# Performance work log

Hardware: AMD Instinct MI355X
Metric: run time of the kernel (lower is better)

The kernel has to match this reference:

```python
import jax, jax.numpy as jnp
import numpy as np

FP8_MAX = 448.0  # finfo(float8_e4m3fn).max

def setup_inputs() -> dict:
    key = jax.random.key(0)
    k_x, k_w, k_b = jax.random.split(key, 3)
    B, S, D_IN, D_OUT = 4, 2048, 4096, 16384
    x = jax.random.normal(k_x, (B, S, D_IN), dtype=jnp.float32)
    # Build an fp8-quantized weight exactly as FP8WeightOnlyLinear.from_linear does:
    w = jax.random.normal(k_w, (D_OUT, D_IN), dtype=jnp.float32) * 0.02
    amax = jnp.max(jnp.abs(w))
    scale = jnp.where(amax > 0, amax / FP8_MAX, 1.0)
    # round-trip through float8_e4m3fn so stored values are true fp8 codes
    w_fp8 = jnp.clip(w / scale, -FP8_MAX, FP8_MAX).astype(jnp.float8_e4m3fn)
    weight_fp8 = w_fp8.astype(jnp.float32)  # fp8-representable values, held in fp32
    weight_scale = scale.reshape(1).astype(jnp.float32)
    bias = jax.random.normal(k_b, (D_OUT,), dtype=jnp.float32) * 0.01
    return {"x": x, "weight_fp8": weight_fp8, "weight_scale": weight_scale, "bias": bias}

def reference(x, weight_fp8, weight_scale, bias):
    # w = weight_fp8.to(x.dtype) * weight_scale ; out = x @ w.T + bias
    w = weight_fp8.astype(x.dtype) * weight_scale.astype(x.dtype)  # [D_OUT, D_IN]
    out = jnp.einsum('bsd,od->bso', x, w) + bias.astype(x.dtype)
    return out
```

## Files before the change

### kernel.cpp

```cpp
#include <hip/hip_runtime.h>
#include <stdint.h>

typedef unsigned int u32;
using i32x4 = __attribute__((ext_vector_type(4))) int;

#define GLD_LDS16(SRC, DST)                                      \
  __builtin_amdgcn_global_load_lds(                              \
      (const __attribute__((address_space(1))) void*)(SRC),      \
      (__attribute__((address_space(3))) void*)(DST), 16, 0, 0)

#define SCHED0() __builtin_amdgcn_sched_barrier(0)
#define BAR()    __builtin_amdgcn_s_barrier()
#define PRIO(x)  __builtin_amdgcn_s_setprio(x)

__global__ __launch_bounds__(256)
void quant_rows(const float* __restrict__ x, const float* __restrict__ w,
                signed char* __restrict__ xq, signed char* __restrict__ wq,
                float* __restrict__ sx, float* __restrict__ sw,
                int Mrows, int totRows, int K) {
  __shared__ float red[4];
  for (int row = blockIdx.x; row < totRows; row += gridDim.x) {
    const bool isx = row < Mrows;
    const float* src = isx ? x + (size_t)row * K : w + (size_t)(row - Mrows) * K;
    const float4* s4 = reinterpret_cast<const float4*>(src) + threadIdx.x * 4;
    float4 v[4];
#pragma unroll
    for (int g = 0; g < 4; ++g) v[g] = s4[g];
    float am = 0.f;
#pragma unroll
    for (int g = 0; g < 4; ++g)
      am = fmaxf(am, fmaxf(fmaxf(fabsf(v[g].x), fabsf(v[g].y)),
                           fmaxf(fabsf(v[g].z), fabsf(v[g].w))));
#pragma unroll
    for (int m = 1; m <= 32; m <<= 1) am = fmaxf(am, __shfl_xor(am, m));
    if ((threadIdx.x & 63) == 0) red[threadIdx.x >> 6] = am;
    __syncthreads();
    am = fmaxf(fmaxf(red[0], red[1]), fmaxf(red[2], red[3]));
    const float s   = am > 0.f ? am * (1.f / 127.f) : 1.f;
    const float inv = am > 0.f ? 127.f / am : 0.f;
    u32 pk[4];
#pragma unroll
    for (int g = 0; g < 4; ++g) {
      const float* vp = reinterpret_cast<const float*>(&v[g]);
      u32 p = 0;
#pragma unroll
      for (int e = 0; e < 4; ++e) {
        int q = (int)rintf(vp[e] * inv);
        q = q < -127 ? -127 : (q > 127 ? 127 : q);
        p |= ((u32)(q & 0xff)) << (8 * e);
      }
      pk[g] = p;
    }
    signed char* dst = (isx ? xq + (size_t)row * K : wq + (size_t)(row - Mrows) * K)
                       + threadIdx.x * 16;
    *reinterpret_cast<uint4*>(dst) = make_uint4(pk[0], pk[1], pk[2], pk[3]);
    if (threadIdx.x == 0) { if (isx) sx[row] = s; else sw[row - Mrows] = s; }
    __syncthreads();
  }
}

__global__ __launch_bounds__(512, 2)
void gemm_i8_bk128(const signed char* __restrict__ A,
                   const signed char* __restrict__ B,
                   const float* __restrict__ sx,
                   const float* __restrict__ sw,
                   const float* __restrict__ wscale_p,
                   const float* __restrict__ bias,
                   float* __restrict__ C,
                   int Nn, int Kk, int NT) {
  __shared__ signed char lds[2][2][256 * 128];

  const int tid  = threadIdx.x;
  const int lane = tid & 63;
  const int wave = tid >> 6;
  const int wr = wave >> 2;
  const int wc = wave & 3;

  const int bid = blockIdx.x;
  const int cpx = gridDim.x >> 3;
  const int wg  = (bid & 7) * cpx + (bid >> 3);
  const int mt = wg / NT, nt = wg % NT;
  const int m0 = mt * 256, n0 = nt * 256;

  const int srow = lane >> 3;
  const int ss   = (lane & 7) ^ (srow & 7);
  const int r16  = lane & 15;
  const int kq   = lane >> 4;

  const signed char* ga = A + ((size_t)m0 + wave * 32 + srow) * Kk + ss * 16;
  const signed char* gb = B + ((size_t)n0 + wave * 32 + srow) * Kk + ss * 16;

  const int aoff = (wr * 128 + r16) * 128 + ((kq ^ (r16 & 7)) << 4);
  const int boff = (wc * 64  + r16) * 128 + ((kq ^ (r16 & 7)) << 4);

  i32x4 acc[8][4];
#pragma unroll
  for (int i = 0; i < 8; ++i)
#pragma unroll
    for (int j = 0; j < 4; ++j)
      acc[i][j] = (i32x4){0, 0, 0, 0};

  i32x4 afA[4], afB[4];
  i32x4 bP[4], bQ[4];

#define STAGE128(bfi_, op_, kt_) do {                                           \
    const signed char* _g = ((op_) ? gb : ga) + (size_t)(kt_) * 128;            \
    signed char* _d = &lds[bfi_][op_][wave * 32 * 128];                         \
    GLD_LDS16(_g,                    _d);                                       \
    GLD_LDS16(_g + (size_t)8  * Kk,  _d + 1024);                                \
    GLD_LDS16(_g + (size_t)16 * Kk,  _d + 2048);                                \
    GLD_LDS16(_g + (size_t)24 * Kk,  _d + 3072);                                \
  } while (0)

#define LDFA(AF_, la_, mh_, ks_) do {                                           \
    _Pragma("unroll") for (int _i = 0; _i < 4; ++_i)                            \
      AF_[_i] = *reinterpret_cast<const i32x4*>(                                \
          (la_) + ((aoff + ((mh_) * 4 + _i) * 2048) ^ ((ks_) << 6)));           \
  } while (0)

#define LDFB(BF_, lb_, ks_) do {                                                \
    _Pragma("unroll") for (int _n = 0; _n < 4; ++_n)                            \
      BF_[_n] = *reinterpret_cast<const i32x4*>(                                \
          (lb_) + ((boff + _n * 2048) ^ ((ks_) << 6)));                         \
  } while (0)

#define MFMAC(mh_, AF_, BF_)                                                    \
  _Pragma("unroll") for (int i = 0; i < 4; ++i)                                 \
  _Pragma("unroll") for (int n = 0; n < 4; ++n)                                 \
    acc[(mh_) * 4 + i][n] = __builtin_amdgcn_mfma_i32_16x16x64_i8(              \
        AF_[i], BF_[n], acc[(mh_) * 4 + i][n], 0, 0, 0)

  const int KT = Kk >> 7;

  STAGE128(0, 0, 0); STAGE128(0, 1, 0);
  STAGE128(1, 0, 1); STAGE128(1, 1, 1);
  asm volatile("s_waitcnt vmcnt(8)" ::: "memory");
  SCHED0(); BAR(); SCHED0();
  LDFA(afA, (const signed char*)&lds[0][0][0], 0, 0);
  LDFB(bP,  (const signed char*)&lds[0][1][0], 0);
  LDFB(bQ,  (const signed char*)&lds[0][1][0], 1);

#define TILE128(t_, CUR_) do {                                                  \
    const signed char* laC = &lds[CUR_][0][0];                                  \
    const signed char* laN = &lds[(CUR_) ^ 1][0][0];                            \
    const signed char* lbN = &lds[(CUR_) ^ 1][1][0];                            \
    const int kt2 = ((t_) + 2 < KT) ? (t_) + 2 : KT - 1;                        \
                                                                        \
    SCHED0(); BAR(); SCHED0();                                                  \
    LDFA(afB, laC, 1, 0);                                                       \
    PRIO(1); MFMAC(0, afA, bP); PRIO(0);                       \
    LDFA(afA, laC, 0, 1);                                                       \
    STAGE128(CUR_, 1, kt2);                                                     \
    PRIO(1); MFMAC(1, afB, bP); PRIO(0);                       \
    LDFA(afB, laC, 1, 1);                                                       \
    SCHED0();                                                                   \
    asm volatile("s_waitcnt vmcnt(4)" ::: "memory");                            \
                                                                        \
    SCHED0(); BAR(); SCHED0();                                                  \
    PRIO(1); MFMAC(0, afA, bQ); PRIO(0);                       \
    LDFA(afA, laN, 0, 0);                                                       \
    LDFB(bP, lbN, 0);                                                           \
    STAGE128(CUR_, 0, kt2);                                                     \
    PRIO(1); MFMAC(1, afB, bQ); PRIO(0);                       \
    LDFB(bQ, lbN, 1);                                \
  } while (0)

  for (int t = 0; t < KT; t += 2) {
    TILE128(t,     0);
    TILE128(t + 1, 1);
  }

  const float wsc = wscale_p[0];
  float cw[4], bv[4];
#pragma unroll
  for (int ni = 0; ni < 4; ++ni) {
    const int col = n0 + wc * 64 + ni * 16 + r16;
    cw[ni] = sw[col] * wsc;
    bv[ni] = bias[col];
  }
#pragma unroll
  for (int mi = 0; mi < 8; ++mi) {
#pragma unroll
    for (int r = 0; r < 4; ++r) {
      const int row = m0 + wr * 128 + mi * 16 + kq * 4 + r;
      const float sxr = sx[row];
      float* cp = C + (size_t)row * Nn + (n0 + wc * 64 + r16);
#pragma unroll
      for (int ni = 0; ni < 4; ++ni)
        cp[ni * 16] = (float)acc[mi][ni][r] * (sxr * cw[ni]) + bv[ni];
    }
  }
#undef STAGE128
#undef LDFA
#undef LDFB
#undef MFMAC
#undef TILE128
}

extern "C" void kernel_launch(void* const* d_in, const int* in_sizes, int n_in,
                              void* d_out, int out_size, void* d_ws, size_t ws_size,
                              hipStream_t stream) {
  (void)n_in; (void)out_size; (void)ws_size;
  const float* x  = (const float*)d_in[0];
  const float* w  = (const float*)d_in[1];
  const float* sc = (const float*)d_in[2];
  const float* bs = (const float*)d_in[3];
  float* out = (float*)d_out;

  const int N = in_sizes[3];
  const int K = in_sizes[1] / N;
  const int M = in_sizes[0] / K;

  signed char* xq = (signed char*)d_ws;
  signed char* wq = xq + (size_t)M * K;
  float* sxp = (float*)(wq + (size_t)N * K);
  float* swp = sxp + M;

  quant_rows<<<M + N, 256, 0, stream>>>(x, w, xq, wq, sxp, swp, M, M + N, K);

  const int NT = N / 256;
  const int nwg = (M / 256) * NT;
  gemm_i8_bk128<<<nwg, 512, 0, stream>>>(xq, wq, sxp, swp, sc, bs, out, N, K, NT);
}
```

Baseline: 629.0 us.

## Replace interleaved LDS/MFMA ping-pong with bulk fragment read then MFMA burst

The GEMM main loop drops the fine-grained interleaving of LDS fragment reads, MFMA groups, global-to-LDS staging and priority toggles. Each K-tile now reads all 24 A/B fragments up front, issues all 64 MFMAs in one burst, and then stages the next tiles with a single barrier per tile. This cuts barriers and setprio overhead and simplifies scheduling. In exchange it holds more registers for fragments and loses overlap between LDS reads and MFMA within a wave, so it relies on the two co-resident workgroups to hide latency.

Result: slower. 644.4 us (+2.4%).

```diff
diff --git a/kernel.cpp b/kernel.cpp
--- a/kernel.cpp
+++ b/kernel.cpp
@@ -11,7 +11,6 @@
 
 #define SCHED0() __builtin_amdgcn_sched_barrier(0)
 #define BAR()    __builtin_amdgcn_s_barrier()
-#define PRIO(x)  __builtin_amdgcn_s_setprio(x)
 
 __global__ __launch_bounds__(256)
 void quant_rows(const float* __restrict__ x, const float* __restrict__ w,
@@ -60,14 +59,14 @@
 }
 
 __global__ __launch_bounds__(512, 2)
-void gemm_i8_bk128(const signed char* __restrict__ A,
-                   const signed char* __restrict__ B,
-                   const float* __restrict__ sx,
-                   const float* __restrict__ sw,
-                   const float* __restrict__ wscale_p,
-                   const float* __restrict__ bias,
-                   float* __restrict__ C,
-                   int Nn, int Kk, int NT) {
+void gemm_i8_deep(const signed char* __restrict__ A,
+                  const signed char* __restrict__ B,
+                  const float* __restrict__ sx,
+                  const float* __restrict__ sw,
+                  const float* __restrict__ wscale_p,
+                  const float* __restrict__ bias,
+                  float* __restrict__ C,
+                  int Nn, int Kk, int NT) {
   __shared__ signed char lds[2][2][256 * 128];
 
   const int tid  = threadIdx.x;
@@ -100,8 +99,8 @@
     for (int j = 0; j < 4; ++j)
       acc[i][j] = (i32x4){0, 0, 0, 0};
 
-  i32x4 afA[4], afB[4];
-  i32x4 bP[4], bQ[4];
+  i32x4 af[16];
+  i32x4 bf[8];
 
 #define STAGE128(bfi_, op_, kt_) do {                                           \
     const signed char* _g = ((op_) ? gb : ga) + (size_t)(kt_) * 128;            \
@@ -112,62 +111,66 @@
     GLD_LDS16(_g + (size_t)24 * Kk,  _d + 3072);                                \
   } while (0)
 
-#define LDFA(AF_, la_, mh_, ks_) do {                                           \
-    _Pragma("unroll") for (int _i = 0; _i < 4; ++_i)                            \
-      AF_[_i] = *reinterpret_cast<const i32x4*>(                                \
-          (la_) + ((aoff + ((mh_) * 4 + _i) * 2048) ^ ((ks_) << 6)));           \
-  } while (0)
-
-#define LDFB(BF_, lb_, ks_) do {                                                \
-    _Pragma("unroll") for (int _n = 0; _n < 4; ++_n)                            \
-      BF_[_n] = *reinterpret_cast<const i32x4*>(                                \
-          (lb_) + ((boff + _n * 2048) ^ ((ks_) << 6)));                         \
-  } while (0)
-
-#define MFMAC(mh_, AF_, BF_)                                                    \
-  _Pragma("unroll") for (int i = 0; i < 4; ++i)                                 \
-  _Pragma("unroll") for (int n = 0; n < 4; ++n)                                 \
-    acc[(mh_) * 4 + i][n] = __builtin_amdgcn_mfma_i32_16x16x64_i8(              \
-        AF_[i], BF_[n], acc[(mh_) * 4 + i][n], 0, 0, 0)
+#define READ24(la_, lb_) do {                                                   \
+    const signed char* _la0 = (la_) + aoff;                                     \
+    const signed char* _la1 = (la_) + (aoff ^ 64);                              \
+    const signed char* _lb0 = (lb_) + boff;                                     \
+    const signed char* _lb1 = (lb_) + (boff ^ 64);                              \
+    _Pragma("unroll") for (int _n = 0; _n < 4; ++_n)                            \
+      bf[_n]      = *reinterpret_cast<const i32x4*>(_lb0 + _n * 2048);          \
+    _Pragma("unroll") for (int _i = 0; _i < 4; ++_i)                            \
+      af[_i]      = *reinterpret_cast<const i32x4*>(_la0 + _i * 2048);          \
+    _Pragma("unroll") for (int _i = 0; _i < 4; ++_i)                            \
+      af[4 + _i]  = *reinterpret_cast<const i32x4*>(_la0 + (4 + _i) * 2048);    \
+    _Pragma("unroll") for (int _n = 0; _n < 4; ++_n)                            \
+      bf[4 + _n]  = *reinterpret_cast<const i32x4*>(_lb1 + _n * 2048);          \
+    _Pragma("unroll") for (int _i = 0; _i < 4; ++_i)                            \
+      af[8 + _i]  = *reinterpret_cast<const i32x4*>(_la1 + _i * 2048);          \
+    _Pragma("unroll") for (int _i = 0; _i < 4; ++_i)                            \
+      af[12 + _i] = *reinterpret_cast<const i32x4*>(_la1 + (4 + _i) * 2048);    \
+  } while (0)
+
+#define MFMA64() do {                                                           \
+    _Pragma("unroll") for (int _i = 0; _i < 4; ++_i)                            \
+    _Pragma("unroll") for (int _n = 0; _n < 4; ++_n)                            \
+      acc[_i][_n] = __builtin_amdgcn_mfma_i32_16x16x64_i8(                      \
+          af[_i], bf[_n], acc[_i][_n], 0, 0, 0);                                \
+    _Pragma("unroll") for (int _i = 0; _i < 4; ++_i)                            \
+    _Pragma("unroll") for (int _n = 0; _n < 4; ++_n)                            \
+      acc[4 + _i][_n] = __builtin_amdgcn_mfma_i32_16x16x64_i8(                  \
+          af[4 + _i], bf[_n], acc[4 + _i][_n], 0, 0, 0);                        \
+    _Pragma("unroll") for (int _i = 0; _i < 4; ++_i)                            \
+    _Pragma("unroll") for (int _n = 0; _n < 4; ++_n)                            \
+      acc[_i][_n] = __builtin_amdgcn_mfma_i32_16x16x64_i8(                      \
+          af[8 + _i], bf[4 + _n], acc[_i][_n], 0, 0, 0);                        \
+    _Pragma("unroll") for (int _i = 0; _i < 4; ++_i)                            \
+    _Pragma("unroll") for (int _n = 0; _n < 4; ++_n)                            \
+      acc[4 + _i][_n] = __builtin_amdgcn_mfma_i32_16x16x64_i8(                  \
+          af[12 + _i], bf[4 + _n], acc[4 + _i][_n], 0, 0, 0);                   \
+  } while (0)
 
   const int KT = Kk >> 7;
 
   STAGE128(0, 0, 0); STAGE128(0, 1, 0);
   STAGE128(1, 0, 1); STAGE128(1, 1, 1);
   asm volatile("s_waitcnt vmcnt(8)" ::: "memory");
-  SCHED0(); BAR(); SCHED0();
-  LDFA(afA, (const signed char*)&lds[0][0][0], 0, 0);
-  LDFB(bP,  (const signed char*)&lds[0][1][0], 0);
-  LDFB(bQ,  (const signed char*)&lds[0][1][0], 1);
-
-#define TILE128(t_, CUR_) do {                                                  \
-    const signed char* laC = &lds[CUR_][0][0];                                  \
-    const signed char* laN = &lds[(CUR_) ^ 1][0][0];                            \
-    const signed char* lbN = &lds[(CUR_) ^ 1][1][0];                            \
+
+#define TILE(t_, CUR_) do {                                                     \
     const int kt2 = ((t_) + 2 < KT) ? (t_) + 2 : KT - 1;                        \
-                                                                        \
     SCHED0(); BAR(); SCHED0();                                                  \
-    LDFA(afB, laC, 1, 0);                                                       \
-    PRIO(1); MFMAC(0, afA, bP); PRIO(0);                       \
-    LDFA(afA, laC, 0, 1);                                                       \
+    READ24((const signed char*)&lds[CUR_][0][0],                                \
+           (const signed char*)&lds[CUR_][1][0]);                               \
+    SCHED0();                                                                   \
+    MFMA64();                                                                   \
+    SCHED0();                                                                   \
+    STAGE128(CUR_, 0, kt2);                                                     \
     STAGE128(CUR_, 1, kt2);                                                     \
-    PRIO(1); MFMAC(1, afB, bP); PRIO(0);                       \
-    LDFA(afB, laC, 1, 1);                                                       \
-    SCHED0();                                                                   \
-    asm volatile("s_waitcnt vmcnt(4)" ::: "memory");                            \
-                                                                        \
-    SCHED0(); BAR(); SCHED0();                                                  \
-    PRIO(1); MFMAC(0, afA, bQ); PRIO(0);                       \
-    LDFA(afA, laN, 0, 0);                                                       \
-    LDFB(bP, lbN, 0);                                                           \
-    STAGE128(CUR_, 0, kt2);                                                     \
-    PRIO(1); MFMAC(1, afB, bQ); PRIO(0);                       \
-    LDFB(bQ, lbN, 1);                                \
+    asm volatile("s_waitcnt vmcnt(8)" ::: "memory");   \
   } while (0)
 
   for (int t = 0; t < KT; t += 2) {
-    TILE128(t,     0);
-    TILE128(t + 1, 1);
+    TILE(t,     0);
+    TILE(t + 1, 1);
   }
 
   const float wsc = wscale_p[0];
@@ -191,10 +194,9 @@
     }
   }
 #undef STAGE128
-#undef LDFA
-#undef LDFB
-#undef MFMAC
-#undef TILE128
+#undef READ24
+#undef MFMA64
+#undef TILE
 }
 
 extern "C" void kernel_launch(void* const* d_in, const int* in_sizes, int n_in,
@@ -220,5 +222,5 @@
 
   const int NT = N / 256;
   const int nwg = (M / 256) * NT;
-  gemm_i8_bk128<<<nwg, 512, 0, stream>>>(xq, wq, sxp, swp, sc, bs, out, N, K, NT);
+  gemm_i8_deep<<<nwg, 512, 0, stream>>>(xq, wq, sxp, swp, sc, bs, out, N, K, NT);
 }
```

## Load B operand directly from global into registers, stage only A in LDS

Applied to the files above, without the earlier changes.

The GEMM now loads B fragments from global memory straight into registers, double-buffered across k-tiles, while only the A operand goes through LDS. This halves LDS footprint and LDS read traffic. The block-to-tile mapping is hardcoded so each XCD owns a band of N tiles with all 32 M tiles, and the s_setprio hints are removed. The risks are uncoalesced 16-byte global loads of B that are duplicated across the two wave rows. The mapping also assumes M/256=32 and N/256=64, so it only holds for this problem shape.

Result: slower. 995.6 us (+58.3%).

```diff
diff --git a/kernel.cpp b/kernel.cpp
--- a/kernel.cpp
+++ b/kernel.cpp
@@ -11,7 +11,6 @@
 
 #define SCHED0() __builtin_amdgcn_sched_barrier(0)
 #define BAR()    __builtin_amdgcn_s_barrier()
-#define PRIO(x)  __builtin_amdgcn_s_setprio(x)
 
 __global__ __launch_bounds__(256)
 void quant_rows(const float* __restrict__ x, const float* __restrict__ w,
@@ -60,15 +59,15 @@
 }
 
 __global__ __launch_bounds__(512, 2)
-void gemm_i8_bk128(const signed char* __restrict__ A,
-                   const signed char* __restrict__ B,
-                   const float* __restrict__ sx,
-                   const float* __restrict__ sw,
-                   const float* __restrict__ wscale_p,
-                   const float* __restrict__ bias,
-                   float* __restrict__ C,
-                   int Nn, int Kk, int NT) {
-  __shared__ signed char lds[2][2][256 * 128];
+void gemm_i8_bdir(const signed char* __restrict__ A,
+                  const signed char* __restrict__ B,
+                  const float* __restrict__ sx,
+                  const float* __restrict__ sw,
+                  const float* __restrict__ wscale_p,
+                  const float* __restrict__ bias,
+                  float* __restrict__ C,
+                  int Nn, int Kk) {
+  __shared__ signed char lds[2][256 * 128];
 
   const int tid  = threadIdx.x;
   const int lane = tid & 63;
@@ -77,9 +76,10 @@
   const int wc = wave & 3;
 
   const int bid = blockIdx.x;
-  const int cpx = gridDim.x >> 3;
-  const int wg  = (bid & 7) * cpx + (bid >> 3);
-  const int mt = wg / NT, nt = wg % NT;
+  const int xcd = bid & 7;
+  const int j   = bid >> 3;
+  const int nt  = xcd * 8 + (j >> 5);
+  const int mt  = j & 31;
   const int m0 = mt * 256, n0 = nt * 256;
 
   const int srow = lane >> 3;
@@ -88,86 +88,76 @@
   const int kq   = lane >> 4;
 
   const signed char* ga = A + ((size_t)m0 + wave * 32 + srow) * Kk + ss * 16;
-  const signed char* gb = B + ((size_t)n0 + wave * 32 + srow) * Kk + ss * 16;
+  const signed char* gBb = B + ((size_t)n0 + wc * 64 + r16) * Kk + (kq << 4);
 
   const int aoff = (wr * 128 + r16) * 128 + ((kq ^ (r16 & 7)) << 4);
-  const int boff = (wc * 64  + r16) * 128 + ((kq ^ (r16 & 7)) << 4);
 
   i32x4 acc[8][4];
 #pragma unroll
   for (int i = 0; i < 8; ++i)
 #pragma unroll
-    for (int j = 0; j < 4; ++j)
-      acc[i][j] = (i32x4){0, 0, 0, 0};
+    for (int jj = 0; jj < 4; ++jj)
+      acc[i][jj] = (i32x4){0, 0, 0, 0};
 
   i32x4 afA[4], afB[4];
-  i32x4 bP[4], bQ[4];
-
-#define STAGE128(bfi_, op_, kt_) do {                                           \
-    const signed char* _g = ((op_) ? gb : ga) + (size_t)(kt_) * 128;            \
-    signed char* _d = &lds[bfi_][op_][wave * 32 * 128];                         \
+  i32x4 bfP[8], bfQ[8];
+
+#define STAGEA(bfi_, kt_) do {                                                  \
+    const signed char* _g = ga + (size_t)(kt_) * 128;                           \
+    signed char* _d = &lds[bfi_][wave * 32 * 128];                              \
     GLD_LDS16(_g,                    _d);                                       \
     GLD_LDS16(_g + (size_t)8  * Kk,  _d + 1024);                                \
     GLD_LDS16(_g + (size_t)16 * Kk,  _d + 2048);                                \
     GLD_LDS16(_g + (size_t)24 * Kk,  _d + 3072);                                \
   } while (0)
 
+#define LOADB(BF_, kt_) do {                                                    \
+    const signed char* _b = gBb + (size_t)(kt_) * 128;                          \
+    _Pragma("unroll") for (int _n = 0; _n < 4; ++_n) {                          \
+      BF_[_n]     = *reinterpret_cast<const i32x4*>(_b + (size_t)(_n * 16) * Kk);      \
+      BF_[4 + _n] = *reinterpret_cast<const i32x4*>(_b + (size_t)(_n * 16) * Kk + 64); \
+    } } while (0)
+
 #define LDFA(AF_, la_, mh_, ks_) do {                                           \
     _Pragma("unroll") for (int _i = 0; _i < 4; ++_i)                            \
       AF_[_i] = *reinterpret_cast<const i32x4*>(                                \
           (la_) + ((aoff + ((mh_) * 4 + _i) * 2048) ^ ((ks_) << 6)));           \
   } while (0)
 
-#define LDFB(BF_, lb_, ks_) do {                                                \
-    _Pragma("unroll") for (int _n = 0; _n < 4; ++_n)                            \
-      BF_[_n] = *reinterpret_cast<const i32x4*>(                                \
-          (lb_) + ((boff + _n * 2048) ^ ((ks_) << 6)));                         \
+#define MFMAC(mh_, AF_, BF_, kb_)                                               \
+  _Pragma("unroll") for (int _i = 0; _i < 4; ++_i)                              \
+  _Pragma("unroll") for (int _n = 0; _n < 4; ++_n)                              \
+    acc[(mh_) * 4 + _i][_n] = __builtin_amdgcn_mfma_i32_16x16x64_i8(            \
+        AF_[_i], BF_[(kb_) * 4 + _n], acc[(mh_) * 4 + _i][_n], 0, 0, 0)
+
+  const int KT = Kk >> 7;
+
+  STAGEA(0, 0);
+  LOADB(bfP, 0);
+  STAGEA(1, 1);
+
+#define TILE(t_, CUR_, BF_, BFN_) do {                                          \
+    const signed char* laC = &lds[CUR_][0];                                     \
+    const int kt1 = ((t_) + 1 < KT) ? (t_) + 1 : KT - 1;                        \
+    const int kt2 = ((t_) + 2 < KT) ? (t_) + 2 : KT - 1;                        \
+    asm volatile("s_waitcnt vmcnt(4)" ::: "memory");      \
+    SCHED0(); BAR(); SCHED0();                                                  \
+    LOADB(BFN_, kt1);                             \
+    LDFA(afA, laC, 0, 0);                                                       \
+    MFMAC(0, afA, BF_, 0);                                     \
+    LDFA(afB, laC, 1, 0);                                                       \
+    MFMAC(1, afB, BF_, 0);                                     \
+    LDFA(afA, laC, 0, 1);                                                       \
+    MFMAC(0, afA, BF_, 1);                                     \
+    LDFA(afB, laC, 1, 1);                                                       \
+    MFMAC(1, afB, BF_, 1);                                     \
+    SCHED0(); BAR(); SCHED0();                      \
+    STAGEA(CUR_, kt2);                                  \
   } while (0)
 
-#define MFMAC(mh_, AF_, BF_)                                                    \
-  _Pragma("unroll") for (int i = 0; i < 4; ++i)                                 \
-  _Pragma("unroll") for (int n = 0; n < 4; ++n)                                 \
-    acc[(mh_) * 4 + i][n] = __builtin_amdgcn_mfma_i32_16x16x64_i8(              \
-        AF_[i], BF_[n], acc[(mh_) * 4 + i][n], 0, 0, 0)
-
-  const int KT = Kk >> 7;
-
-  STAGE128(0, 0, 0); STAGE128(0, 1, 0);
-  STAGE128(1, 0, 1); STAGE128(1, 1, 1);
-  asm volatile("s_waitcnt vmcnt(8)" ::: "memory");
-  SCHED0(); BAR(); SCHED0();
-  LDFA(afA, (const signed char*)&lds[0][0][0], 0, 0);
-  LDFB(bP,  (const signed char*)&lds[0][1][0], 0);
-  LDFB(bQ,  (const signed char*)&lds[0][1][0], 1);
-
-#define TILE128(t_, CUR_) do {                                                  \
-    const signed char* laC = &lds[CUR_][0][0];                                  \
-    const signed char* laN = &lds[(CUR_) ^ 1][0][0];                            \
-    const signed char* lbN = &lds[(CUR_) ^ 1][1][0];                            \
-    const int kt2 = ((t_) + 2 < KT) ? (t_) + 2 : KT - 1;                        \
-                                                                        \
-    SCHED0(); BAR(); SCHED0();                                                  \
-    LDFA(afB, laC, 1, 0);                                                       \
-    PRIO(1); MFMAC(0, afA, bP); PRIO(0);                       \
-    LDFA(afA, laC, 0, 1);                                                       \
-    STAGE128(CUR_, 1, kt2);                                                     \
-    PRIO(1); MFMAC(1, afB, bP); PRIO(0);                       \
-    LDFA(afB, laC, 1, 1);                                                       \
-    SCHED0();                                                                   \
-    asm volatile("s_waitcnt vmcnt(4)" ::: "memory");                            \
-                                                                        \
-    SCHED0(); BAR(); SCHED0();                                                  \
-    PRIO(1); MFMAC(0, afA, bQ); PRIO(0);                       \
-    LDFA(afA, laN, 0, 0);                                                       \
-    LDFB(bP, lbN, 0);                                                           \
-    STAGE128(CUR_, 0, kt2);                                                     \
-    PRIO(1); MFMAC(1, afB, bQ); PRIO(0);                       \
-    LDFB(bQ, lbN, 1);                                \
-  } while (0)
-
   for (int t = 0; t < KT; t += 2) {
-    TILE128(t,     0);
-    TILE128(t + 1, 1);
+    TILE(t,     0, bfP, bfQ);
+    TILE(t + 1, 1, bfQ, bfP);
   }
 
   const float wsc = wscale_p[0];
@@ -190,11 +180,11 @@
         cp[ni * 16] = (float)acc[mi][ni][r] * (sxr * cw[ni]) + bv[ni];
     }
   }
-#undef STAGE128
+#undef STAGEA
+#undef LOADB
 #undef LDFA
-#undef LDFB
 #undef MFMAC
-#undef TILE128
+#undef TILE
 }
 
 extern "C" void kernel_launch(void* const* d_in, const int* in_sizes, int n_in,
@@ -218,7 +208,6 @@
 
   quant_rows<<<M + N, 256, 0, stream>>>(x, w, xq, wq, sxp, swp, M, M + N, K);
 
-  const int NT = N / 256;
-  const int nwg = (M / 256) * NT;
-  gemm_i8_bk128<<<nwg, 512, 0, stream>>>(xq, wq, sxp, swp, sc, bs, out, N, K, NT);
+  const int nwg = (M / 256) * (N / 256);
+  gemm_i8_bdir<<<nwg, 512, 0, stream>>>(xq, wq, sxp, swp, sc, bs, out, N, K);
 }
```

## Shrink GEMM tile to 128x128 with 4-wave workgroups and rebalanced MFMA schedule

Applied to the files above, without the earlier changes.

Replaces the 256x256 tile, 8-wave int8 GEMM with a 128x128 tile, 4-wave kernel. Each wave keeps a 64x64 accumulator, and the in-loop schedule is reworked so MFMA batches interleave with LDS fragment loads and global-to-LDS staging. Smaller tiles halve LDS use per workgroup and give more workgroups. In exchange, arithmetic intensity per tile drops, which doubles global and L2 traffic for A and B.

Result: slower. 814.8 us (+29.5%).

```diff
diff --git a/kernel.cpp b/kernel.cpp
--- a/kernel.cpp
+++ b/kernel.cpp
@@ -59,28 +59,28 @@
   }
 }
 
-__global__ __launch_bounds__(512, 2)
-void gemm_i8_bk128(const signed char* __restrict__ A,
-                   const signed char* __restrict__ B,
-                   const float* __restrict__ sx,
-                   const float* __restrict__ sw,
-                   const float* __restrict__ wscale_p,
-                   const float* __restrict__ bias,
-                   float* __restrict__ C,
-                   int Nn, int Kk, int NT) {
-  __shared__ signed char lds[2][2][256 * 128];
+__global__ __launch_bounds__(256, 2)
+void gemm_i8_2wg(const signed char* __restrict__ A,
+                 const signed char* __restrict__ B,
+                 const float* __restrict__ sx,
+                 const float* __restrict__ sw,
+                 const float* __restrict__ wscale_p,
+                 const float* __restrict__ bias,
+                 float* __restrict__ C,
+                 int Nn, int Kk, int NT) {
+  __shared__ signed char lds[2][2][128 * 128];
 
   const int tid  = threadIdx.x;
   const int lane = tid & 63;
   const int wave = tid >> 6;
-  const int wr = wave >> 2;
-  const int wc = wave & 3;
+  const int wr = wave >> 1;
+  const int wc = wave & 1;
 
   const int bid = blockIdx.x;
   const int cpx = gridDim.x >> 3;
   const int wg  = (bid & 7) * cpx + (bid >> 3);
   const int mt = wg / NT, nt = wg % NT;
-  const int m0 = mt * 256, n0 = nt * 256;
+  const int m0 = mt * 128, n0 = nt * 128;
 
   const int srow = lane >> 3;
   const int ss   = (lane & 7) ^ (srow & 7);
@@ -90,12 +90,12 @@
   const signed char* ga = A + ((size_t)m0 + wave * 32 + srow) * Kk + ss * 16;
   const signed char* gb = B + ((size_t)n0 + wave * 32 + srow) * Kk + ss * 16;
 
-  const int aoff = (wr * 128 + r16) * 128 + ((kq ^ (r16 & 7)) << 4);
-  const int boff = (wc * 64  + r16) * 128 + ((kq ^ (r16 & 7)) << 4);
-
-  i32x4 acc[8][4];
-#pragma unroll
-  for (int i = 0; i < 8; ++i)
+  const int aoff = (wr * 64 + r16) * 128 + ((kq ^ (r16 & 7)) << 4);
+  const int boff = (wc * 64 + r16) * 128 + ((kq ^ (r16 & 7)) << 4);
+
+  i32x4 acc[4][4];
+#pragma unroll
+  for (int i = 0; i < 4; ++i)
 #pragma unroll
     for (int j = 0; j < 4; ++j)
       acc[i][j] = (i32x4){0, 0, 0, 0};
@@ -103,7 +103,7 @@
   i32x4 afA[4], afB[4];
   i32x4 bP[4], bQ[4];
 
-#define STAGE128(bfi_, op_, kt_) do {                                           \
+#define STAGE1(bfi_, op_, kt_) do {                                             \
     const signed char* _g = ((op_) ? gb : ga) + (size_t)(kt_) * 128;            \
     signed char* _d = &lds[bfi_][op_][wave * 32 * 128];                         \
     GLD_LDS16(_g,                    _d);                                       \
@@ -112,10 +112,10 @@
     GLD_LDS16(_g + (size_t)24 * Kk,  _d + 3072);                                \
   } while (0)
 
-#define LDFA(AF_, la_, mh_, ks_) do {                                           \
+#define LDFA(AF_, la_, ks_) do {                                                \
     _Pragma("unroll") for (int _i = 0; _i < 4; ++_i)                            \
       AF_[_i] = *reinterpret_cast<const i32x4*>(                                \
-          (la_) + ((aoff + ((mh_) * 4 + _i) * 2048) ^ ((ks_) << 6)));           \
+          (la_) + ((aoff + _i * 2048) ^ ((ks_) << 6)));                         \
   } while (0)
 
 #define LDFB(BF_, lb_, ks_) do {                                                \
@@ -124,50 +124,53 @@
           (lb_) + ((boff + _n * 2048) ^ ((ks_) << 6)));                         \
   } while (0)
 
-#define MFMAC(mh_, AF_, BF_)                                                    \
-  _Pragma("unroll") for (int i = 0; i < 4; ++i)                                 \
-  _Pragma("unroll") for (int n = 0; n < 4; ++n)                                 \
-    acc[(mh_) * 4 + i][n] = __builtin_amdgcn_mfma_i32_16x16x64_i8(              \
-        AF_[i], BF_[n], acc[(mh_) * 4 + i][n], 0, 0, 0)
+#define MFMA16(AF_, BF_)                                                        \
+  _Pragma("unroll") for (int _i = 0; _i < 4; ++_i)                              \
+  _Pragma("unroll") for (int _n = 0; _n < 4; ++_n)                              \
+    acc[_i][_n] = __builtin_amdgcn_mfma_i32_16x16x64_i8(                        \
+        AF_[_i], BF_[_n], acc[_i][_n], 0, 0, 0)
+
+#define MFMA8(AF_, BF_, nlo_)                                                   \
+  _Pragma("unroll") for (int _i = 0; _i < 4; ++_i)                              \
+  _Pragma("unroll") for (int _n = 0; _n < 2; ++_n)                              \
+    acc[_i][(nlo_) + _n] = __builtin_amdgcn_mfma_i32_16x16x64_i8(               \
+        AF_[_i], BF_[(nlo_) + _n], acc[_i][(nlo_) + _n], 0, 0, 0)
 
   const int KT = Kk >> 7;
 
-  STAGE128(0, 0, 0); STAGE128(0, 1, 0);
-  STAGE128(1, 0, 1); STAGE128(1, 1, 1);
+  STAGE1(0, 0, 0); STAGE1(0, 1, 0);
+  STAGE1(1, 0, 1); STAGE1(1, 1, 1);
   asm volatile("s_waitcnt vmcnt(8)" ::: "memory");
   SCHED0(); BAR(); SCHED0();
-  LDFA(afA, (const signed char*)&lds[0][0][0], 0, 0);
+  LDFA(afA, (const signed char*)&lds[0][0][0], 0);
   LDFB(bP,  (const signed char*)&lds[0][1][0], 0);
   LDFB(bQ,  (const signed char*)&lds[0][1][0], 1);
 
-#define TILE128(t_, CUR_) do {                                                  \
+#define TILE(t_, CUR_) do {                                                     \
     const signed char* laC = &lds[CUR_][0][0];                                  \
     const signed char* laN = &lds[(CUR_) ^ 1][0][0];                            \
     const signed char* lbN = &lds[(CUR_) ^ 1][1][0];                            \
     const int kt2 = ((t_) + 2 < KT) ? (t_) + 2 : KT - 1;                        \
                                                                         \
     SCHED0(); BAR(); SCHED0();                                                  \
-    LDFA(afB, laC, 1, 0);                                                       \
-    PRIO(1); MFMAC(0, afA, bP); PRIO(0);                       \
-    LDFA(afA, laC, 0, 1);                                                       \
-    STAGE128(CUR_, 1, kt2);                                                     \
-    PRIO(1); MFMAC(1, afB, bP); PRIO(0);                       \
-    LDFA(afB, laC, 1, 1);                                                       \
+    LDFA(afB, laC, 1);                                               \
+    STAGE1(CUR_, 1, kt2);                        \
+    PRIO(1); MFMA16(afA, bP); PRIO(0);                             \
     SCHED0();                                                                   \
-    asm volatile("s_waitcnt vmcnt(4)" ::: "memory");                            \
+    asm volatile("s_waitcnt vmcnt(4)" ::: "memory");       \
                                                                         \
     SCHED0(); BAR(); SCHED0();                                                  \
-    PRIO(1); MFMAC(0, afA, bQ); PRIO(0);                       \
-    LDFA(afA, laN, 0, 0);                                                       \
+    PRIO(1); MFMA8(afB, bQ, 0); PRIO(0);                   \
+    LDFA(afA, laN, 0);                                        \
     LDFB(bP, lbN, 0);                                                           \
-    STAGE128(CUR_, 0, kt2);                                                     \
-    PRIO(1); MFMAC(1, afB, bQ); PRIO(0);                       \
-    LDFB(bQ, lbN, 1);                                \
+    STAGE1(CUR_, 0, kt2);                                      \
+    PRIO(1); MFMA8(afB, bQ, 2); PRIO(0);                   \
+    LDFB(bQ, lbN, 1);                               \
   } while (0)
 
   for (int t = 0; t < KT; t += 2) {
-    TILE128(t,     0);
-    TILE128(t + 1, 1);
+    TILE(t,     0);
+    TILE(t + 1, 1);
   }
 
   const float wsc = wscale_p[0];
@@ -179,10 +182,10 @@
     bv[ni] = bias[col];
   }
 #pragma unroll
-  for (int mi = 0; mi < 8; ++mi) {
+  for (int mi = 0; mi < 4; ++mi) {
 #pragma unroll
     for (int r = 0; r < 4; ++r) {
-      const int row = m0 + wr * 128 + mi * 16 + kq * 4 + r;
+      const int row = m0 + wr * 64 + mi * 16 + kq * 4 + r;
       const float sxr = sx[row];
       float* cp = C + (size_t)row * Nn + (n0 + wc * 64 + r16);
 #pragma unroll
@@ -190,11 +193,12 @@
         cp[ni * 16] = (float)acc[mi][ni][r] * (sxr * cw[ni]) + bv[ni];
     }
   }
-#undef STAGE128
+#undef STAGE1
 #undef LDFA
 #undef LDFB
-#undef MFMAC
-#undef TILE128
+#undef MFMA16
+#undef MFMA8
+#undef TILE
 }
 
 extern "C" void kernel_launch(void* const* d_in, const int* in_sizes, int n_in,
@@ -218,7 +222,7 @@
 
   quant_rows<<<M + N, 256, 0, stream>>>(x, w, xq, wq, sxp, swp, M, M + N, K);
 
-  const int NT = N / 256;
-  const int nwg = (M / 256) * NT;
-  gemm_i8_bk128<<<nwg, 512, 0, stream>>>(xq, wq, sxp, swp, sc, bs, out, N, K, NT);
+  const int NT = N / 128;
+  const int nwg = (M / 128) * NT;
+  gemm_i8_2wg<<<nwg, 256, 0, stream>>>(xq, wq, sxp, swp, sc, bs, out, N, K, NT);
 }
```
